# Optimization experiments

Hardware: AMD Instinct MI355X
Metric: run time of the kernel (lower is better)

Reference implementation:

```python
import jax, jax.numpy as jnp
import numpy as np

# Tri-plane query (coords=None path) of GrowingGeneratorTriplane:
#   vol = cat([yz bcast over x, xz bcast over y, xy bcast over z], -1)  # [1,X,Y,Z,3C]
#   out = sigmoid(Linear(3C->1)(vol))                                   # [1,1,X,Y,Z]
# Because the MLP (mlp_layers=0) is a single linear layer, we apply the
# three weight chunks to each plane first and broadcast-add the scalar
# partial sums, which is mathematically identical to materializing the
# concatenated volume but avoids the ~0.8 GB intermediate.

C = 32   # feat_dim
R = 128  # X = Y = Z grid resolution


def setup_inputs() -> dict:
    key = jax.random.key(0)
    k1, k2, k3, k4, k5 = jax.random.split(key, 5)
    yz_feat = jax.random.normal(k1, (1, C, R, R), dtype=jnp.float32)  # [1,C,Y,Z]
    xz_feat = jax.random.normal(k2, (1, C, R, R), dtype=jnp.float32)  # [1,C,X,Z]
    xy_feat = jax.random.normal(k3, (1, C, R, R), dtype=jnp.float32)  # [1,C,X,Y]
    W = jax.random.normal(k4, (3 * C, 1), dtype=jnp.float32)          # Linear(96,1) weight (in,out)
    b = jax.random.normal(k5, (1,), dtype=jnp.float32)                # Linear bias
    return {"yz_feat": yz_feat, "xz_feat": xz_feat, "xy_feat": xy_feat, "W": W, "b": b}


def reference(yz_feat, xz_feat, xy_feat, W, b):
    c = yz_feat.shape[1]
    w_yz, w_xz, w_xy = W[:c, 0], W[c:2 * c, 0], W[2 * c:, 0]
    # per-plane partial linear outputs (scalar channel)
    p_yz = jnp.einsum('bcyz,c->byz', yz_feat, w_yz)  # [B,Y,Z]
    p_xz = jnp.einsum('bcxz,c->bxz', xz_feat, w_xz)  # [B,X,Z]
    p_xy = jnp.einsum('bcxy,c->bxy', xy_feat, w_xy)  # [B,X,Y]
    # broadcast-sum over the full volume: [B,X,Y,Z]
    logits = p_yz[:, None, :, :] + p_xz[:, :, None, :] + p_xy[:, :, :, None] + b[0]
    return jax.nn.sigmoid(logits)[:, None]  # [B,1,X,Y,Z]
```

## Files before the change

### kernel.cpp

```cpp
#include <hip/hip_runtime.h>
#include <hip/hip_bf16.h>


#define C 32
#define R 128
#define PLANE (R * R)

#define BX 8
#define BY 8
#define BZ 64

__global__ __launch_bounds__(256) void triplane_fused_kernel(
        const float* __restrict__ yz,
        const float* __restrict__ xz,
        const float* __restrict__ xy,
        const float* __restrict__ W,
        const float* __restrict__ bptr,
        float* __restrict__ out) {
    __shared__ float pyz[BY][BZ];
    __shared__ float pxz[BX][BZ];
    __shared__ float pxy[BX][BY];
    __shared__ float w[3 * C];

    const int bid = blockIdx.x;
    const int zh = bid & 1;
    const int yt = (bid >> 1) & 15;
    const int xt = bid >> 5;
    const int x0 = xt * BX, y0 = yt * BY, z0 = zh * BZ;
    const int t = threadIdx.x;

    if (t < 3 * C) w[t] = W[t];
    __syncthreads();

    for (int e = t; e < BY * BZ; e += 256) {
        int yi = e >> 6, zi = e & 63;
        const float* src = yz + (y0 + yi) * R + z0 + zi;
        float acc = 0.0f;
#pragma unroll
        for (int c = 0; c < C; ++c) acc += src[c * PLANE] * w[c];
        pyz[yi][zi] = acc;
    }
    for (int e = t; e < BX * BZ; e += 256) {
        int xi = e >> 6, zi = e & 63;
        const float* src = xz + (x0 + xi) * R + z0 + zi;
        float acc = 0.0f;
#pragma unroll
        for (int c = 0; c < C; ++c) acc += src[c * PLANE] * w[C + c];
        pxz[xi][zi] = acc;
    }
    if (t < BX * BY) {
        int xi = t >> 3, yi = t & 7;
        const float* src = xy + (x0 + xi) * R + (y0 + yi);
        float acc = 0.0f;
#pragma unroll
        for (int c = 0; c < C; ++c) acc += src[c * PLANE] * w[2 * C + c];
        pxy[xi][yi] = acc;
    }
    const float bb = bptr[0];
    __syncthreads();

    const int z16 = t & 15;
    const int r0 = t >> 4;
#pragma unroll
    for (int it = 0; it < 4; ++it) {
        int r = r0 + 16 * it;
        int xi = r >> 3, yi = r & 7;
        float base = pxy[xi][yi] + bb;
        float4 a = *reinterpret_cast<const float4*>(&pyz[yi][z16 * 4]);
        float4 c4 = *reinterpret_cast<const float4*>(&pxz[xi][z16 * 4]);
        float4 o;
        o.x = 1.0f / (1.0f + __expf(-(a.x + c4.x + base)));
        o.y = 1.0f / (1.0f + __expf(-(a.y + c4.y + base)));
        o.z = 1.0f / (1.0f + __expf(-(a.z + c4.z + base)));
        o.w = 1.0f / (1.0f + __expf(-(a.w + c4.w + base)));
        *reinterpret_cast<float4*>(out + (x0 + xi) * PLANE + (y0 + yi) * R + z0 + z16 * 4) = o;
    }
}

extern "C" void kernel_launch(void* const* d_in, const int* in_sizes, int n_in,
                              void* d_out, int out_size, void* d_ws, size_t ws_size,
                              hipStream_t stream) {
    const float* yz = (const float*)d_in[0];
    const float* xz = (const float*)d_in[1];
    const float* xy = (const float*)d_in[2];
    const float* W  = (const float*)d_in[3];
    const float* b  = (const float*)d_in[4];
    float* out = (float*)d_out;

    triplane_fused_kernel<<<512, 256, 0, stream>>>(yz, xz, xy, W, b, out);
}
```

Measured before the change: 12.71 us.

## Switch to cubic 16^3 tiles with rcp sigmoid and nontemporal stores

Changes the block tile from 8x8x64 to 16x16x16, so each block computes one partial sum per thread for each of the three planes. This balances the plane projection work across threads, and the per-block plane reads now cover 256 pixels each rather than 512+512+64. The sigmoid division is replaced with the hardware reciprocal, and output stores become nontemporal. The cost is shorter contiguous output rows (64 bytes along z instead of 256), which may reduce write coalescing.

```diff
diff --git a/kernel.cpp b/kernel.cpp
--- a/kernel.cpp
+++ b/kernel.cpp
@@ -6,9 +6,9 @@
 #define R 128
 #define PLANE (R * R)
 
-#define BX 8
-#define BY 8
-#define BZ 64
+#define BT 16
+
+typedef float f32x4 __attribute__((ext_vector_type(4)));
 
 __global__ __launch_bounds__(256) void triplane_fused_kernel(
         const float* __restrict__ yz,
@@ -17,63 +17,64 @@
         const float* __restrict__ W,
         const float* __restrict__ bptr,
         float* __restrict__ out) {
-    __shared__ float pyz[BY][BZ];
-    __shared__ float pxz[BX][BZ];
-    __shared__ float pxy[BX][BY];
+    __shared__ float pyz[BT][BT];
+    __shared__ float pxz[BT][BT];
+    __shared__ float pxy[BT][BT];
     __shared__ float w[3 * C];
 
     const int bid = blockIdx.x;
-    const int zh = bid & 1;
-    const int yt = (bid >> 1) & 15;
-    const int xt = bid >> 5;
-    const int x0 = xt * BX, y0 = yt * BY, z0 = zh * BZ;
+    const int zt = bid & 7;
+    const int yt = (bid >> 3) & 7;
+    const int xt = bid >> 6;
+    const int x0 = xt * BT, y0 = yt * BT, z0 = zt * BT;
     const int t = threadIdx.x;
 
     if (t < 3 * C) w[t] = W[t];
     __syncthreads();
 
-    for (int e = t; e < BY * BZ; e += 256) {
-        int yi = e >> 6, zi = e & 63;
-        const float* src = yz + (y0 + yi) * R + z0 + zi;
+    const int i0 = t >> 4;
+    const int i1 = t & 15;
+
+    {
+        const float* src = yz + (y0 + i0) * R + (z0 + i1);
         float acc = 0.0f;
 #pragma unroll
         for (int c = 0; c < C; ++c) acc += src[c * PLANE] * w[c];
-        pyz[yi][zi] = acc;
+        pyz[i0][i1] = acc;
     }
-    for (int e = t; e < BX * BZ; e += 256) {
-        int xi = e >> 6, zi = e & 63;
-        const float* src = xz + (x0 + xi) * R + z0 + zi;
+    {
+        const float* src = xz + (x0 + i0) * R + (z0 + i1);
         float acc = 0.0f;
 #pragma unroll
         for (int c = 0; c < C; ++c) acc += src[c * PLANE] * w[C + c];
-        pxz[xi][zi] = acc;
+        pxz[i0][i1] = acc;
     }
-    if (t < BX * BY) {
-        int xi = t >> 3, yi = t & 7;
-        const float* src = xy + (x0 + xi) * R + (y0 + yi);
+    {
+        const float* src = xy + (x0 + i0) * R + (y0 + i1);
         float acc = 0.0f;
 #pragma unroll
         for (int c = 0; c < C; ++c) acc += src[c * PLANE] * w[2 * C + c];
-        pxy[xi][yi] = acc;
+        pxy[i0][i1] = acc;
     }
     const float bb = bptr[0];
     __syncthreads();
 
-    const int z16 = t & 15;
-    const int r0 = t >> 4;
+    const int z4 = t & 3;
+    const int yi = (t >> 2) & 15;
+    const int xi0 = t >> 6;
 #pragma unroll
     for (int it = 0; it < 4; ++it) {
-        int r = r0 + 16 * it;
-        int xi = r >> 3, yi = r & 7;
+        int xi = xi0 + 4 * it;
         float base = pxy[xi][yi] + bb;
-        float4 a = *reinterpret_cast<const float4*>(&pyz[yi][z16 * 4]);
-        float4 c4 = *reinterpret_cast<const float4*>(&pxz[xi][z16 * 4]);
-        float4 o;
-        o.x = 1.0f / (1.0f + __expf(-(a.x + c4.x + base)));
-        o.y = 1.0f / (1.0f + __expf(-(a.y + c4.y + base)));
-        o.z = 1.0f / (1.0f + __expf(-(a.z + c4.z + base)));
-        o.w = 1.0f / (1.0f + __expf(-(a.w + c4.w + base)));
-        *reinterpret_cast<float4*>(out + (x0 + xi) * PLANE + (y0 + yi) * R + z0 + z16 * 4) = o;
+        f32x4 a = *reinterpret_cast<const f32x4*>(&pyz[yi][z4 * 4]);
+        f32x4 c4 = *reinterpret_cast<const f32x4*>(&pxz[xi][z4 * 4]);
+        f32x4 o;
+        o.x = __builtin_amdgcn_rcpf(1.0f + __expf(-(a.x + c4.x + base)));
+        o.y = __builtin_amdgcn_rcpf(1.0f + __expf(-(a.y + c4.y + base)));
+        o.z = __builtin_amdgcn_rcpf(1.0f + __expf(-(a.z + c4.z + base)));
+        o.w = __builtin_amdgcn_rcpf(1.0f + __expf(-(a.w + c4.w + base)));
+        __builtin_nontemporal_store(o,
+            reinterpret_cast<f32x4*>(out + (x0 + xi) * PLANE + (y0 + yi) * R + z0 + z4 * 4));
     }
 }
 
```

Result: faster. 10.41 us (-18.1%).
